# Performance work log

Hardware: AMD Instinct MI355X
Metric: run time of the kernel (lower is better)

The kernel has to match this reference:

```python
import jax, jax.numpy as jnp
import numpy as np

SCALAR = 8.0
FIRE_RATE = 0.5


def _depthwise3x3(x, k3x3):
    # x: [B,C,H,W]; k3x3: [3,3] applied identically to every channel (groups=C)
    C = x.shape[1]
    kern = jnp.broadcast_to(k3x3, (C, 1, 3, 3)).astype(x.dtype)
    return jax.lax.conv_general_dilated(
        x, kern, window_strides=(1, 1), padding='SAME',
        dimension_numbers=('NCHW', 'OIHW', 'NCHW'), feature_group_count=C)


def _norm_per_channel(G):
    # torch loop: per-channel global (over batch+spatial) min/max shift+scale
    mn = jnp.abs(jnp.min(G, axis=(0, 2, 3), keepdims=True))  # [1,C,1,1]
    mx = jnp.abs(jnp.max(G, axis=(0, 2, 3), keepdims=True))
    div = mn + mx
    return (G + mn) / jnp.where(div == 0, jnp.ones_like(div), div)


def _percieve(x):
    # angle = 0: sobel_x = dx/8, sobel_y = dx.T/8
    dx = jnp.asarray(np.outer([1, 2, 1], [-1, 0, 1]) / SCALAR, jnp.float32)
    dy = dx.T
    lap = jnp.asarray(np.array([[0, 1, 0], [1, -4, 1], [0, 1, 0]]) / SCALAR, jnp.float32)
    G_x = _depthwise3x3(x, dx)
    G_y = _depthwise3x3(x, dy)
    G_l = _depthwise3x3(x, lap)
    G_i = x  # identity 3x3 kernel == identity
    G_xn = _norm_per_channel(G_x)
    G_yn = _norm_per_channel(G_y)
    G_mag = jnp.sqrt(G_xn * G_xn + G_yn * G_yn)
    return jnp.concatenate([G_i, G_l, G_mag], axis=1)  # [B,3C,H,W]


def _living_mask(x):
    alpha = x[:, 3:4]  # [B,1,H,W]
    pooled = jax.lax.reduce_window(alpha, -jnp.inf, jax.lax.max,
                                   (1, 1, 3, 3), (1, 1, 1, 1), 'SAME')
    return pooled > 0.1


def reference(x, w1, b1, w2, mask_rand):
    pre_life = _living_mask(x)
    y = jax.lax.stop_gradient(_percieve(x))  # percieve runs under no_grad
    h = jax.nn.relu(jnp.einsum('bchw,oc->bohw', y, w1) + b1[None, :, None, None])
    dx = jnp.einsum('bchw,oc->bohw', h, w2)
    fire = (mask_rand <= FIRE_RATE).astype(x.dtype)  # [B,1,H,W]
    x_new = x + dx * fire
    post_life = _living_mask(x_new)
    life = (pre_life & post_life).astype(x.dtype)
    return x_new * life


def setup_inputs() -> dict:
    key = jax.random.key(0)
    ks = jax.random.split(key, 5)
    B, C, H, W, HID = 32, 16, 256, 256, 128
    return {
        'x': jax.random.normal(ks[0], (B, C, H, W), jnp.float32),
        'w1': jax.random.normal(ks[1], (HID, 3 * C), jnp.float32) * 0.05,
        'b1': jax.random.normal(ks[2], (HID,), jnp.float32) * 0.05,
        'w2': jax.random.normal(ks[3], (C, HID), jnp.float32) * 0.05,
        'mask_rand': jax.random.uniform(ks[4], (B, 1, H, W), jnp.float32),
    }
```

## Files before the change

kernel.cpp:

```cpp
#include <hip/hip_runtime.h>

#define B 32
#define C 16
#define H 256
#define W 256
#define HID 128
#define HW (H*W)
#define MROWS 32
#define NMM 4096

typedef __attribute__((ext_vector_type(8))) _Float16 f16x8;
typedef __attribute__((ext_vector_type(4))) _Float16 f16x4;
typedef __attribute__((ext_vector_type(4))) float f32x4;

__device__ __forceinline__ unsigned fkey(float f){
  unsigned u = __float_as_uint(f);
  return (u & 0x80000000u) ? ~u : (u | 0x80000000u);
}
__device__ __forceinline__ float fkeyinv(unsigned k){
  unsigned u = (k & 0x80000000u) ? (k & 0x7FFFFFFFu) : ~k;
  return __uint_as_float(u);
}
__device__ __forceinline__ int pk2(_Float16 a, _Float16 b){
  union { _Float16 h[2]; int i; } u; u.h[0]=a; u.h[1]=b; return u.i;
}
__device__ __forceinline__ int physc(int c, int key){
  return (c < 8) ? (c ^ (key & 7)) : (8 + ((c & 3) ^ (key & 3)));
}

__global__ __launch_bounds__(64) void k_pm(
    const float* __restrict__ x, const float* __restrict__ w1,
    const float* __restrict__ w2, unsigned* __restrict__ mm,
    _Float16* __restrict__ w1kh, _Float16* __restrict__ w1kl,
    _Float16* __restrict__ w1k1h, _Float16* __restrict__ w1k1l,
    _Float16* __restrict__ w2h)
{
  const int tid = threadIdx.x;
  if (blockIdx.x >= NMM){
    int e = (blockIdx.x - NMM)*64 + tid;
    if (e < 4096){
      int j = e & 7, l = (e >> 3) & 63, ot = e >> 9;
      float v = w1[(16*ot + (l & 15))*48 + 8*(l >> 4) + j];
      _Float16 h = (_Float16)v;
      w1kh[e] = h; w1kl[e] = (_Float16)(v - (float)h);
    } else if (e < 6144){
      int e2 = e - 4096;
      int j = e2 & 3, l = (e2 >> 2) & 63, ot = e2 >> 8;
      float v = w1[(16*ot + (l & 15))*48 + 32 + 4*(l >> 4) + j];
      _Float16 h = (_Float16)v;
      w1k1h[e2] = h; w1k1l[e2] = (_Float16)(v - (float)h);
    } else if (e < 8192){
      int e2 = e - 6144;
      int j = e2 & 7, l = (e2 >> 3) & 63, s = e2 >> 9;
      w2h[e2] = (_Float16)w2[(l & 15)*128 + 32*s + 8*(l >> 4) + j];
    }
    return;
  }
  int chunk = blockIdx.x & 7, bc = blockIdx.x >> 3, c = bc & 15;
  const float* p = x + (size_t)bc * HW;
  const int j4 = tid * 4;
  const int i0 = chunk * MROWS;

  float Aw[6], Bw[6], Cw[6];
  auto loadrow = [&](int row, float* wv){
    float4 v = *(const float4*)(p + (size_t)row*W + j4);
    float l = __shfl(v.w, tid - 1);
    float r = __shfl(v.x, tid + 1);
    if (tid == 0)  l = 0.f;
    if (tid == 63) r = 0.f;
    wv[0]=l; wv[1]=v.x; wv[2]=v.y; wv[3]=v.z; wv[4]=v.w; wv[5]=r;
  };
  if (i0 > 0) loadrow(i0-1, Aw);
  else { for (int t=0;t<6;++t) Aw[t]=0.f; }
  loadrow(i0, Bw);

  float gxmn = 1e30f, gxmx = -1e30f, gymn = 1e30f, gymx = -1e30f;
  for (int r = 0; r < MROWS; ++r){
    int ipr = i0 + r + 1;
    if (ipr < H) loadrow(ipr, Cw);
    else { for (int t=0;t<6;++t) Cw[t]=0.f; }
    #pragma unroll
    for (int t = 0; t < 4; ++t){
      float gx = (Aw[t+2]-Aw[t] + 2.f*(Bw[t+2]-Bw[t]) + Cw[t+2]-Cw[t]) * 0.125f;
      float gy = (Cw[t]-Aw[t] + 2.f*(Cw[t+1]-Aw[t+1]) + Cw[t+2]-Aw[t+2]) * 0.125f;
      gxmn = fminf(gxmn, gx); gxmx = fmaxf(gxmx, gx);
      gymn = fminf(gymn, gy); gymx = fmaxf(gymx, gy);
    }
    #pragma unroll
    for (int t = 0; t < 6; ++t){ Aw[t] = Bw[t]; Bw[t] = Cw[t]; }
  }
  for (int off = 32; off; off >>= 1){
    gxmn = fminf(gxmn, __shfl_down(gxmn, off));
    gxmx = fmaxf(gxmx, __shfl_down(gxmx, off));
    gymn = fminf(gymn, __shfl_down(gymn, off));
    gymx = fmaxf(gymx, __shfl_down(gymx, off));
  }
  if (tid == 0){
    atomicMin(&mm[c],      fkey(gxmn));
    atomicMin(&mm[16+c],   fkey(gymn));
    atomicMax(&mm[32+c],   fkey(gxmx));
    atomicMax(&mm[48+c],   fkey(gymx));
  }
}

__global__ __launch_bounds__(64) void k_main(
    const float* __restrict__ x, const float* __restrict__ mrand,
    const unsigned* __restrict__ mm,
    const _Float16* __restrict__ w1kh, const _Float16* __restrict__ w1kl,
    const _Float16* __restrict__ w1k1h, const _Float16* __restrict__ w1k1l,
    const _Float16* __restrict__ w2h, const float* __restrict__ w2f,
    const float* __restrict__ b1,
    float* __restrict__ out, float* __restrict__ alpha_new,
    unsigned char* __restrict__ premask)
{
  __shared__ __align__(16) _Float16 yl[64][104];
  __shared__ float amn_x[16], inv_x[16], amn_y[16], inv_y[16];

  const int tid = threadIdx.x;
  const int blk = blockIdx.x;
  const int quarter = blk & 3;
  const int rowid = blk >> 2;
  const int i = rowid & 255, b = rowid >> 8;
  const int j0 = quarter << 6;
  const int q = tid >> 4, n16 = tid & 15;

  if (tid < 16){
    int c = tid;
    float mn = fabsf(fkeyinv(mm[c]));
    float mx = fabsf(fkeyinv(mm[32+c]));
    float dv = mn + mx;
    amn_x[c] = mn; inv_x[c] = (dv == 0.f) ? 1.f : 1.f/dv;
    mn = fabsf(fkeyinv(mm[16+c]));
    mx = fabsf(fkeyinv(mm[48+c]));
    dv = mn + mx;
    amn_y[c] = mn; inv_y[c] = (dv == 0.f) ? 1.f : 1.f/dv;
  }

  {
    const float* xb = x + (size_t)b * C * HW;
    const int j = j0 + tid;
    const int key = tid & 15;
    const int im = i-1, ipp = i+1;
    const bool iu = im >= 0, id = ipp < H, jl = j > 0, jr = j < W-1;
    #pragma unroll
    for (int hp = 0; hp < 2; ++hp){
      float xv[8], lv[8], mv[8];
      #pragma unroll
      for (int cc = 0; cc < 8; ++cc){
        const int c = hp*8 + cc;
        const float* pc = xb + (size_t)c * HW;
        const float* r0 = pc + (size_t)im*W;
        const float* r1 = pc + (size_t)i*W;
        const float* r2 = pc + (size_t)ipp*W;
        float v00 = (iu&&jl) ? r0[j-1] : 0.f;
        float v01 =  iu      ? r0[j]   : 0.f;
        float v02 = (iu&&jr) ? r0[j+1] : 0.f;
        float v10 =  jl      ? r1[j-1] : 0.f;
        float v11 =            r1[j];
        float v12 =  jr      ? r1[j+1] : 0.f;
        float v20 = (id&&jl) ? r2[j-1] : 0.f;
        float v21 =  id      ? r2[j]   : 0.f;
        float v22 = (id&&jr) ? r2[j+1] : 0.f;
        float gx = (v02 - v00 + 2.f*(v12 - v10) + v22 - v20) * 0.125f;
        float gy = (v20 - v00 + 2.f*(v21 - v01) + v22 - v02) * 0.125f;
        float gl = (v01 + v10 + v12 + v21 - 4.f*v11) * 0.125f;
        float gxn = (gx + amn_x[c]) * inv_x[c];
        float gyn = (gy + amn_y[c]) * inv_y[c];
        xv[cc] = v11;
        lv[cc] = gl;
        mv[cc] = sqrtf(gxn*gxn + gyn*gyn);
        if (hp == 0 && cc == 3){
          float pre3 = fmaxf(fmaxf(fmaxf(v00,v01),fmaxf(v02,v10)),
                       fmaxf(fmaxf(v11,v12),fmaxf(fmaxf(v20,v21),v22)));
          premask[(size_t)b*HW + (size_t)i*W + j] = (pre3 > 0.1f) ? 1 : 0;
        }
      }
      f16x8 vh, vl;
      #pragma unroll
      for (int e = 0; e < 8; ++e){ _Float16 h=(_Float16)xv[e]; vh[e]=h; vl[e]=(_Float16)(xv[e]-(float)h); }
      *(f16x8*)&yl[tid][physc(hp,    key)*8] = vh;
      *(f16x8*)&yl[tid][physc(6+hp,  key)*8] = vl;
      #pragma unroll
      for (int e = 0; e < 8; ++e){ _Float16 h=(_Float16)lv[e]; vh[e]=h; vl[e]=(_Float16)(lv[e]-(float)h); }
      *(f16x8*)&yl[tid][physc(2+hp,  key)*8] = vh;
      *(f16x8*)&yl[tid][physc(8+hp,  key)*8] = vl;
      #pragma unroll
      for (int e = 0; e < 8; ++e){ _Float16 h=(_Float16)mv[e]; vh[e]=h; vl[e]=(_Float16)(mv[e]-(float)h); }
      *(f16x8*)&yl[tid][physc(4+hp,  key)*8] = vh;
      *(f16x8*)&yl[tid][physc(10+hp, key)*8] = vl;
    }
  }

  f16x8 A1h[8], A1l[8];
  #pragma unroll
  for (int ot = 0; ot < 8; ++ot){
    A1h[ot] = *(const f16x8*)(w1kh + ot*512 + tid*8);
    A1l[ot] = *(const f16x8*)(w1kl + ot*512 + tid*8);
  }
  f16x8 A2h[4];
  #pragma unroll
  for (int s = 0; s < 4; ++s)
    A2h[s] = *(const f16x8*)(w2h + s*512 + tid*8);

  const size_t rowbase = (size_t)b*C*HW + (size_t)i*W;
  const size_t abase   = (size_t)b*HW + (size_t)i*W;
  const float* mr_row  = mrand + abase + j0;
  const float* w2r3    = w2f + 3*HID;
  const int srcA = 32*(q&1) + n16;
  const bool hiq = (q >= 2);

  #pragma unroll 1
  for (int g = 0; g < 4; ++g){
    const int pl = g*16 + n16;
    const int key = n16;
    const _Float16* yr = yl[pl];
    f16x8 Bh0 = *(const f16x8*)&yr[physc(q,     key)*8];
    f16x8 Bl0 = *(const f16x8*)&yr[physc(6+q,   key)*8];
    f16x4 Bh1 = *(const f16x4*)&yr[physc(4+(q>>1),  key)*8 + 4*(q&1)];
    f16x4 Bl1 = *(const f16x4*)&yr[physc(10+(q>>1), key)*8 + 4*(q&1)];

    int hh[8][2];
    float partial3 = 0.f;
    #pragma unroll
    for (int ot = 0; ot < 8; ++ot){
      f16x4 A1h1 = *(const f16x4*)(w1k1h + ot*256 + tid*4);
      f16x4 A1l1 = *(const f16x4*)(w1k1l + ot*256 + tid*4);
      f32x4 acc = *(const f32x4*)(b1 + 16*ot + 4*q);
      acc = __builtin_amdgcn_mfma_f32_16x16x32_f16(A1h[ot], Bh0, acc, 0, 0, 0);
      acc = __builtin_amdgcn_mfma_f32_16x16x32_f16(A1h[ot], Bl0, acc, 0, 0, 0);
      acc = __builtin_amdgcn_mfma_f32_16x16x32_f16(A1l[ot], Bh0, acc, 0, 0, 0);
      acc = __builtin_amdgcn_mfma_f32_16x16x32_f16(A1l[ot], Bl0, acc, 0, 0, 0);
      acc = __builtin_amdgcn_mfma_f32_16x16x16f16(A1h1, Bh1, acc, 0, 0, 0);
      acc = __builtin_amdgcn_mfma_f32_16x16x16f16(A1h1, Bl1, acc, 0, 0, 0);
      acc = __builtin_amdgcn_mfma_f32_16x16x16f16(A1l1, Bh1, acc, 0, 0, 0);
      acc = __builtin_amdgcn_mfma_f32_16x16x16f16(A1l1, Bl1, acc, 0, 0, 0);
      float h0 = fmaxf(acc[0],0.f), h1 = fmaxf(acc[1],0.f);
      float h2 = fmaxf(acc[2],0.f), h3 = fmaxf(acc[3],0.f);
      hh[ot][0] = pk2((_Float16)h0, (_Float16)h1);
      hh[ot][1] = pk2((_Float16)h2, (_Float16)h3);
      f32x4 w3 = *(const f32x4*)(w2r3 + 16*ot + 4*q);
      partial3 = fmaf(w3[0],h0, fmaf(w3[1],h1, fmaf(w3[2],h2, fmaf(w3[3],h3, partial3))));
    }
    partial3 += __shfl_xor(partial3, 16);
    partial3 += __shfl_xor(partial3, 32);

    f32x4 d2 = {0.f, 0.f, 0.f, 0.f};
    #pragma unroll
    for (int s = 0; s < 4; ++s){
      int e0 = __shfl(hh[2*s  ][0], srcA),    e1 = __shfl(hh[2*s  ][1], srcA);
      int f0 = __shfl(hh[2*s+1][0], srcA),    f1 = __shfl(hh[2*s+1][1], srcA);
      int g0 = __shfl(hh[2*s  ][0], srcA+16), g1 = __shfl(hh[2*s  ][1], srcA+16);
      int k0 = __shfl(hh[2*s+1][0], srcA+16), k1 = __shfl(hh[2*s+1][1], srcA+16);
      union { int d[4]; f16x8 v; } bh;
      bh.d[0] = hiq ? f0 : e0; bh.d[1] = hiq ? f1 : e1;
      bh.d[2] = hiq ? k0 : g0; bh.d[3] = hiq ? k1 : g1;
      d2 = __builtin_amdgcn_mfma_f32_16x16x32_f16(A2h[s], bh.v, d2, 0, 0, 0);
    }

    const float fire = (mr_row[pl] <= 0.5f) ? 1.f : 0.f;
    float a3v = 0.f;
    #pragma unroll
    for (int r = 0; r < 4; ++r){
      const int c = 4*q + r;
      const size_t idx = rowbase + (size_t)c*HW + (j0 + pl);
      const float xv = x[idx];
      const float dxv = (c == 3) ? partial3 : d2[r];
      const float val = xv + dxv*fire;
      out[idx] = val;
      if (c == 3) a3v = val;
    }
    if (q == 0) alpha_new[abase + j0 + pl] = a3v;
  }
}

__global__ __launch_bounds__(256) void k_life(
    const float* __restrict__ alpha_new,
    const unsigned char* __restrict__ premask,
    float* __restrict__ out)
{
  __shared__ float lds[258];
  const int i = blockIdx.x & 255, b = blockIdx.x >> 8;
  const int j = threadIdx.x;
  const float* an = alpha_new + (size_t)b*HW;
  float m = an[(size_t)i*W + j];
  if (i > 0)   m = fmaxf(m, an[(size_t)(i-1)*W + j]);
  if (i < 255) m = fmaxf(m, an[(size_t)(i+1)*W + j]);
  if (j == 0){ lds[0] = 0.f; lds[257] = 0.f; }
  lds[j+1] = m;
  __syncthreads();
  float pooled = fmaxf(fmaxf(lds[j], lds[j+1]), lds[j+2]);
  bool life = (premask[(size_t)b*HW + (size_t)i*W + j] != 0) && (pooled > 0.1f);
  if (!life){
    size_t px = (size_t)b*C*HW + (size_t)i*W + j;
    #pragma unroll
    for (int c = 0; c < 16; ++c) out[px + (size_t)c*HW] = 0.f;
  }
}

extern "C" void kernel_launch(void* const* d_in, const int* in_sizes, int n_in,
                              void* d_out, int out_size, void* d_ws, size_t ws_size,
                              hipStream_t stream) {
  const float* x  = (const float*)d_in[0];
  const float* w1 = (const float*)d_in[1];
  const float* b1 = (const float*)d_in[2];
  const float* w2 = (const float*)d_in[3];
  const float* mr = (const float*)d_in[4];

  char* ws = (char*)d_ws;
  unsigned* mm          = (unsigned*)ws;
  float* alpha_n        = (float*)(ws + 256);
  unsigned char* pmask  = (unsigned char*)(ws + 256 + 8388608);
  char* wb              = ws + 256 + 8388608 + 2097152;
  _Float16* w1kh  = (_Float16*)(wb);
  _Float16* w1kl  = (_Float16*)(wb + 8192);
  _Float16* w1k1h = (_Float16*)(wb + 16384);
  _Float16* w1k1l = (_Float16*)(wb + 20480);
  _Float16* w2h   = (_Float16*)(wb + 24576);
  float* out = (float*)d_out;

  (void)hipMemsetAsync(mm, 0xFF, 128, stream);
  (void)hipMemsetAsync((char*)mm + 128, 0x00, 128, stream);
  k_pm  <<<NMM + 128, 64, 0, stream>>>(x, w1, w2, mm, w1kh, w1kl,
                                       w1k1h, w1k1l, w2h);
  k_main<<<B*H*4, 64, 0, stream>>>(x, mr, mm, w1kh, w1kl, w1k1h, w1k1l,
                                   w2h, w2, b1, out, alpha_n, pmask);
  k_life<<<B*H, 256, 0, stream>>>(alpha_n, pmask, out);
}
```

Before: 351.3 us.

## Share stencil neighbours via shuffles, cache x in LDS, swizzle block order

Loads only the centre column of each of the three stencil rows and gets the left and right neighbours through wave shuffles. Only lanes 0 and 63 fall back to global loads at the wave edges. Keeps the fp32 x values in an enlarged LDS tile, using a plain XOR swizzle, so the epilogue reads x from LDS instead of reloading it from global memory. It also remaps block indices with a stride-8 swizzle, which changes how blocks map to rows, and it adds LDS per block.

```diff
diff --git a/kernel.cpp b/kernel.cpp
--- a/kernel.cpp
+++ b/kernel.cpp
@@ -23,9 +23,6 @@
 }
 __device__ __forceinline__ int pk2(_Float16 a, _Float16 b){
   union { _Float16 h[2]; int i; } u; u.h[0]=a; u.h[1]=b; return u.i;
-}
-__device__ __forceinline__ int physc(int c, int key){
-  return (c < 8) ? (c ^ (key & 7)) : (8 + ((c & 3) ^ (key & 3)));
 }
 
 __global__ __launch_bounds__(64) void k_pm(
@@ -113,13 +110,14 @@
     float* __restrict__ out, float* __restrict__ alpha_new,
     unsigned char* __restrict__ premask)
 {
-  __shared__ __align__(16) _Float16 yl[64][104];
+  __shared__ __align__(16) _Float16 yl[64][128];
   __shared__ float amn_x[16], inv_x[16], amn_y[16], inv_y[16];
 
   const int tid = threadIdx.x;
   const int blk = blockIdx.x;
-  const int quarter = blk & 3;
-  const int rowid = blk >> 2;
+  const int bswz = (blk & 7)*4096 + (blk >> 3);
+  const int quarter = bswz & 3;
+  const int rowid = bswz >> 2;
   const int i = rowid & 255, b = rowid >> 8;
   const int j0 = quarter << 6;
   const int q = tid >> 4, n16 = tid & 15;
@@ -152,15 +150,24 @@
         const float* r0 = pc + (size_t)im*W;
         const float* r1 = pc + (size_t)i*W;
         const float* r2 = pc + (size_t)ipp*W;
-        float v00 = (iu&&jl) ? r0[j-1] : 0.f;
-        float v01 =  iu      ? r0[j]   : 0.f;
-        float v02 = (iu&&jr) ? r0[j+1] : 0.f;
-        float v10 =  jl      ? r1[j-1] : 0.f;
-        float v11 =            r1[j];
-        float v12 =  jr      ? r1[j+1] : 0.f;
-        float v20 = (id&&jl) ? r2[j-1] : 0.f;
-        float v21 =  id      ? r2[j]   : 0.f;
-        float v22 = (id&&jr) ? r2[j+1] : 0.f;
+        float v01 = iu ? r0[j] : 0.f;
+        float v11 = r1[j];
+        float v21 = id ? r2[j] : 0.f;
+        float v00 = __shfl_up(v01, 1);
+        float v10 = __shfl_up(v11, 1);
+        float v20 = __shfl_up(v21, 1);
+        float v02 = __shfl_down(v01, 1);
+        float v12 = __shfl_down(v11, 1);
+        float v22 = __shfl_down(v21, 1);
+        if (tid == 0){
+          v00 = (iu&&jl) ? r0[j-1] : 0.f;
+          v10 =  jl      ? r1[j-1] : 0.f;
+          v20 = (id&&jl) ? r2[j-1] : 0.f;
+        } else if (tid == 63){
+          v02 = (iu&&jr) ? r0[j+1] : 0.f;
+          v12 =  jr      ? r1[j+1] : 0.f;
+          v22 = (id&&jr) ? r2[j+1] : 0.f;
+        }
         float gx = (v02 - v00 + 2.f*(v12 - v10) + v22 - v20) * 0.125f;
         float gy = (v20 - v00 + 2.f*(v21 - v01) + v22 - v02) * 0.125f;
         float gl = (v01 + v10 + v12 + v21 - 4.f*v11) * 0.125f;
@@ -178,16 +185,23 @@
       f16x8 vh, vl;
       #pragma unroll
       for (int e = 0; e < 8; ++e){ _Float16 h=(_Float16)xv[e]; vh[e]=h; vl[e]=(_Float16)(xv[e]-(float)h); }
-      *(f16x8*)&yl[tid][physc(hp,    key)*8] = vh;
-      *(f16x8*)&yl[tid][physc(6+hp,  key)*8] = vl;
+      *(f16x8*)&yl[tid][((hp     ) ^ key)*8] = vh;
+      *(f16x8*)&yl[tid][((6+hp   ) ^ key)*8] = vl;
       #pragma unroll
       for (int e = 0; e < 8; ++e){ _Float16 h=(_Float16)lv[e]; vh[e]=h; vl[e]=(_Float16)(lv[e]-(float)h); }
-      *(f16x8*)&yl[tid][physc(2+hp,  key)*8] = vh;
-      *(f16x8*)&yl[tid][physc(8+hp,  key)*8] = vl;
+      *(f16x8*)&yl[tid][((2+hp   ) ^ key)*8] = vh;
+      *(f16x8*)&yl[tid][((8+hp   ) ^ key)*8] = vl;
       #pragma unroll
       for (int e = 0; e < 8; ++e){ _Float16 h=(_Float16)mv[e]; vh[e]=h; vl[e]=(_Float16)(mv[e]-(float)h); }
-      *(f16x8*)&yl[tid][physc(4+hp,  key)*8] = vh;
-      *(f16x8*)&yl[tid][physc(10+hp, key)*8] = vl;
+      *(f16x8*)&yl[tid][((4+hp   ) ^ key)*8] = vh;
+      *(f16x8*)&yl[tid][((10+hp  ) ^ key)*8] = vl;
+      #pragma unroll
+      for (int t = 0; t < 2; ++t){
+        union { float f[4]; f16x8 v; } u;
+        #pragma unroll
+        for (int e = 0; e < 4; ++e) u.f[e] = xv[4*t+e];
+        *(f16x8*)&yl[tid][((12+2*hp+t) ^ key)*8] = u.v;
+      }
     }
   }
 
@@ -214,10 +228,10 @@
     const int pl = g*16 + n16;
     const int key = n16;
     const _Float16* yr = yl[pl];
-    f16x8 Bh0 = *(const f16x8*)&yr[physc(q,     key)*8];
-    f16x8 Bl0 = *(const f16x8*)&yr[physc(6+q,   key)*8];
-    f16x4 Bh1 = *(const f16x4*)&yr[physc(4+(q>>1),  key)*8 + 4*(q&1)];
-    f16x4 Bl1 = *(const f16x4*)&yr[physc(10+(q>>1), key)*8 + 4*(q&1)];
+    f16x8 Bh0 = *(const f16x8*)&yr[(( q          ) ^ key)*8];
+    f16x8 Bl0 = *(const f16x8*)&yr[(( 6+q        ) ^ key)*8];
+    f16x4 Bh1 = *(const f16x4*)(&yr[(( 4+(q>>1)  ) ^ key)*8] + 4*(q&1));
+    f16x4 Bl1 = *(const f16x4*)(&yr[((10+(q>>1)  ) ^ key)*8] + 4*(q&1));
 
     int hh[8][2];
     float partial3 = 0.f;
@@ -257,16 +271,16 @@
       d2 = __builtin_amdgcn_mfma_f32_16x16x32_f16(A2h[s], bh.v, d2, 0, 0, 0);
     }
 
+    union { f16x8 v; float f[4]; } xu;
+    xu.v = *(const f16x8*)&yr[((12+q) ^ key)*8];
     const float fire = (mr_row[pl] <= 0.5f) ? 1.f : 0.f;
     float a3v = 0.f;
     #pragma unroll
     for (int r = 0; r < 4; ++r){
       const int c = 4*q + r;
-      const size_t idx = rowbase + (size_t)c*HW + (j0 + pl);
-      const float xv = x[idx];
       const float dxv = (c == 3) ? partial3 : d2[r];
-      const float val = xv + dxv*fire;
-      out[idx] = val;
+      const float val = xu.f[r] + dxv*fire;
+      out[rowbase + (size_t)c*HW + (j0 + pl)] = val;
       if (c == 3) a3v = val;
     }
     if (q == 0) alpha_new[abase + j0 + pl] = a3v;
```

Measured after the change: 407.7 us. +16.1%, slower.

## Stage hidden activations through LDS instead of cross-lane shuffles, swizzle block order

Applied to the files above, without the earlier changes.

The hidden-layer tile between the two MFMA GEMMs is now written to the shared-memory row (reusing the y buffer, widened to 128 halves) and read back as B operands, replacing 16 ds_bpermute shuffles per step. The XOR swizzle is simplified to a plain 4-bit XOR over 16 slots. Block indices are also remapped so that consecutive blocks stride across the grid, which changes how work is spread over XCDs and caches. The extra LDS round trip and the larger shared-memory footprint may cost occupancy, and correctness depends on implicit in-wave ordering of the LDS write and read.

```diff
diff --git a/kernel.cpp b/kernel.cpp
--- a/kernel.cpp
+++ b/kernel.cpp
@@ -20,12 +20,6 @@
 __device__ __forceinline__ float fkeyinv(unsigned k){
   unsigned u = (k & 0x80000000u) ? (k & 0x7FFFFFFFu) : ~k;
   return __uint_as_float(u);
-}
-__device__ __forceinline__ int pk2(_Float16 a, _Float16 b){
-  union { _Float16 h[2]; int i; } u; u.h[0]=a; u.h[1]=b; return u.i;
-}
-__device__ __forceinline__ int physc(int c, int key){
-  return (c < 8) ? (c ^ (key & 7)) : (8 + ((c & 3) ^ (key & 3)));
 }
 
 __global__ __launch_bounds__(64) void k_pm(
@@ -113,13 +107,14 @@
     float* __restrict__ out, float* __restrict__ alpha_new,
     unsigned char* __restrict__ premask)
 {
-  __shared__ __align__(16) _Float16 yl[64][104];
+  __shared__ __align__(16) _Float16 yl[64][128];
   __shared__ float amn_x[16], inv_x[16], amn_y[16], inv_y[16];
 
   const int tid = threadIdx.x;
   const int blk = blockIdx.x;
-  const int quarter = blk & 3;
-  const int rowid = blk >> 2;
+  const int bswz = (blk & 7)*4096 + (blk >> 3);
+  const int quarter = bswz & 3;
+  const int rowid = bswz >> 2;
   const int i = rowid & 255, b = rowid >> 8;
   const int j0 = quarter << 6;
   const int q = tid >> 4, n16 = tid & 15;
@@ -178,16 +173,16 @@
       f16x8 vh, vl;
       #pragma unroll
       for (int e = 0; e < 8; ++e){ _Float16 h=(_Float16)xv[e]; vh[e]=h; vl[e]=(_Float16)(xv[e]-(float)h); }
-      *(f16x8*)&yl[tid][physc(hp,    key)*8] = vh;
-      *(f16x8*)&yl[tid][physc(6+hp,  key)*8] = vl;
+      *(f16x8*)&yl[tid][((hp     ) ^ key)*8] = vh;
+      *(f16x8*)&yl[tid][((6+hp   ) ^ key)*8] = vl;
       #pragma unroll
       for (int e = 0; e < 8; ++e){ _Float16 h=(_Float16)lv[e]; vh[e]=h; vl[e]=(_Float16)(lv[e]-(float)h); }
-      *(f16x8*)&yl[tid][physc(2+hp,  key)*8] = vh;
-      *(f16x8*)&yl[tid][physc(8+hp,  key)*8] = vl;
+      *(f16x8*)&yl[tid][((2+hp   ) ^ key)*8] = vh;
+      *(f16x8*)&yl[tid][((8+hp   ) ^ key)*8] = vl;
       #pragma unroll
       for (int e = 0; e < 8; ++e){ _Float16 h=(_Float16)mv[e]; vh[e]=h; vl[e]=(_Float16)(mv[e]-(float)h); }
-      *(f16x8*)&yl[tid][physc(4+hp,  key)*8] = vh;
-      *(f16x8*)&yl[tid][physc(10+hp, key)*8] = vl;
+      *(f16x8*)&yl[tid][((4+hp   ) ^ key)*8] = vh;
+      *(f16x8*)&yl[tid][((10+hp  ) ^ key)*8] = vl;
     }
   }
 
@@ -206,20 +201,17 @@
   const size_t abase   = (size_t)b*HW + (size_t)i*W;
   const float* mr_row  = mrand + abase + j0;
   const float* w2r3    = w2f + 3*HID;
-  const int srcA = 32*(q&1) + n16;
-  const bool hiq = (q >= 2);
 
   #pragma unroll 1
   for (int g = 0; g < 4; ++g){
     const int pl = g*16 + n16;
     const int key = n16;
-    const _Float16* yr = yl[pl];
-    f16x8 Bh0 = *(const f16x8*)&yr[physc(q,     key)*8];
-    f16x8 Bl0 = *(const f16x8*)&yr[physc(6+q,   key)*8];
-    f16x4 Bh1 = *(const f16x4*)&yr[physc(4+(q>>1),  key)*8 + 4*(q&1)];
-    f16x4 Bl1 = *(const f16x4*)&yr[physc(10+(q>>1), key)*8 + 4*(q&1)];
-
-    int hh[8][2];
+    _Float16* yr = yl[pl];
+    f16x8 Bh0 = *(const f16x8*)&yr[(( q          ) ^ key)*8];
+    f16x8 Bl0 = *(const f16x8*)&yr[(( 6+q        ) ^ key)*8];
+    f16x4 Bh1 = *(const f16x4*)(&yr[(( 4+(q>>1)  ) ^ key)*8] + 4*(q&1));
+    f16x4 Bl1 = *(const f16x4*)(&yr[((10+(q>>1)  ) ^ key)*8] + 4*(q&1));
+
     float partial3 = 0.f;
     #pragma unroll
     for (int ot = 0; ot < 8; ++ot){
@@ -236,10 +228,11 @@
       acc = __builtin_amdgcn_mfma_f32_16x16x16f16(A1l1, Bl1, acc, 0, 0, 0);
       float h0 = fmaxf(acc[0],0.f), h1 = fmaxf(acc[1],0.f);
       float h2 = fmaxf(acc[2],0.f), h3 = fmaxf(acc[3],0.f);
-      hh[ot][0] = pk2((_Float16)h0, (_Float16)h1);
-      hh[ot][1] = pk2((_Float16)h2, (_Float16)h3);
       f32x4 w3 = *(const f32x4*)(w2r3 + 16*ot + 4*q);
       partial3 = fmaf(w3[0],h0, fmaf(w3[1],h1, fmaf(w3[2],h2, fmaf(w3[3],h3, partial3))));
+      f16x4 hv;
+      hv[0]=(_Float16)h0; hv[1]=(_Float16)h1; hv[2]=(_Float16)h2; hv[3]=(_Float16)h3;
+      *(f16x4*)(&yr[(((2*ot + (q>>1)) ^ key)*8) + 4*(q&1)]) = hv;
     }
     partial3 += __shfl_xor(partial3, 16);
     partial3 += __shfl_xor(partial3, 32);
@@ -247,14 +240,8 @@
     f32x4 d2 = {0.f, 0.f, 0.f, 0.f};
     #pragma unroll
     for (int s = 0; s < 4; ++s){
-      int e0 = __shfl(hh[2*s  ][0], srcA),    e1 = __shfl(hh[2*s  ][1], srcA);
-      int f0 = __shfl(hh[2*s+1][0], srcA),    f1 = __shfl(hh[2*s+1][1], srcA);
-      int g0 = __shfl(hh[2*s  ][0], srcA+16), g1 = __shfl(hh[2*s  ][1], srcA+16);
-      int k0 = __shfl(hh[2*s+1][0], srcA+16), k1 = __shfl(hh[2*s+1][1], srcA+16);
-      union { int d[4]; f16x8 v; } bh;
-      bh.d[0] = hiq ? f0 : e0; bh.d[1] = hiq ? f1 : e1;
-      bh.d[2] = hiq ? k0 : g0; bh.d[3] = hiq ? k1 : g1;
-      d2 = __builtin_amdgcn_mfma_f32_16x16x32_f16(A2h[s], bh.v, d2, 0, 0, 0);
+      f16x8 B2 = *(const f16x8*)&yr[((4*s + q) ^ key)*8];
+      d2 = __builtin_amdgcn_mfma_f32_16x16x32_f16(A2h[s], B2, d2, 0, 0, 0);
     }
 
     const float fire = (mr_row[pl] <= 0.5f) ? 1.f : 0.f;
```

Result: faster. 343.0 us (-2.4%).
